# Optimization experiments

Hardware: AMD Instinct MI355X
Metric: run time of the kernel (lower is better)

Reference implementation:

```python
import jax, jax.numpy as jnp
import numpy as np
import math

PHI = (1.0 + math.sqrt(5.0)) / 2.0
LN_EPS = 1e-5


def _carrier_phases(n_heads: int) -> np.ndarray:
    """Reproduce DimensionalHeadManager._allocate carrier phases."""
    base = [k * math.pi / 7.0 for k in range(7)]  # rung base phases
    n_rungs = 7
    raw = []
    remaining = n_heads
    for i in range(n_rungs):
        if i < n_rungs - 1:
            c = max(1, round(n_heads / PHI ** (i + 1)))
            c = min(c, remaining - (n_rungs - 1 - i))
            raw.append(c)
            remaining -= c
        else:
            raw.append(max(1, remaining))
    phases = []
    for rung_idx, count in enumerate(raw):
        for j in range(count):
            phases.append(base[rung_idx] + 2.0 * math.pi / max(count, 1) * j)
    return np.asarray(phases[:n_heads], dtype=np.float32)


def setup_inputs() -> dict:
    key = jax.random.key(0)
    ks = jax.random.split(key, 7)
    B, S, D, H = 2, 2048, 1024, 16
    w_scale = 0.02  # realistic init scale for Linear weights
    x = jax.random.normal(ks[0], (B, S, D), dtype=jnp.float32)
    Wq = jax.random.normal(ks[1], (D, D), dtype=jnp.float32) * w_scale
    Wk = jax.random.normal(ks[2], (D, D), dtype=jnp.float32) * w_scale
    Wv = jax.random.normal(ks[3], (D, D), dtype=jnp.float32) * w_scale
    Wo = jax.random.normal(ks[4], (D, D), dtype=jnp.float32) * w_scale
    Wp = jax.random.normal(ks[5], (D,), dtype=jnp.float32) * w_scale  # W_phase (1,D) flattened
    gamma = jnp.ones((D,), dtype=jnp.float32)
    beta = jnp.zeros((D,), dtype=jnp.float32)
    carrier = jnp.asarray(_carrier_phases(H))  # srl.carrier_freq init
    lam = jnp.float32(0.1)  # lambda_resonance init
    return {"x": x, "Wq": Wq, "Wk": Wk, "Wv": Wv, "Wo": Wo, "Wp": Wp,
            "gamma": gamma, "beta": beta, "carrier": carrier, "lam": lam}


def reference(x, Wq, Wk, Wv, Wo, Wp, gamma, beta, carrier, lam):
    B, S, D = x.shape
    H = carrier.shape[0]
    dh = D // H
    scale = 1.0 / math.sqrt(dh)

    residual = x
    # LayerNorm
    mu = jnp.mean(x, axis=-1, keepdims=True)
    var = jnp.mean((x - mu) ** 2, axis=-1, keepdims=True)
    xn = (x - mu) * jax.lax.rsqrt(var + LN_EPS) * gamma + beta

    # Q/K/V projections (torch Linear: y = x @ W.T), split into heads
    q = jnp.einsum('bsd,ed->bse', xn, Wq).reshape(B, S, H, dh)
    k = jnp.einsum('bsd,ed->bse', xn, Wk).reshape(B, S, H, dh)
    v = jnp.einsum('bsd,ed->bse', xn, Wv).reshape(B, S, H, dh)

    # scalar phase per token, per-head carrier resonance gate
    phase = jnp.einsum('bsd,d->bs', xn, Wp)                       # (B,S)
    head_T = jnp.cos((phase[..., None] - carrier) * 0.5) ** 2     # (B,S,H)

    # attention scores + resonance term R_ij = cos^2((phi_i - phi_j)/2)
    scores = jnp.einsum('bihd,bjhd->bhij', q, k) * scale          # (B,H,S,S)
    R = jnp.cos((phase[:, :, None] - phase[:, None, :]) * 0.5) ** 2  # (B,S,S)
    scores = scores + lam * R[:, None, :, :]

    attn = jax.nn.softmax(scores, axis=-1)
    out = jnp.einsum('bhij,bjhd->bihd', attn, v)                  # (B,S,H,dh)
    out = out * head_T[..., None]                                 # per-head resonance gating
    emergent_energy = jnp.sum(jnp.abs(out))
    y = residual + jnp.einsum('bse,de->bsd', out.reshape(B, S, D), Wo)
    return (y, emergent_energy)
```

## Files before the change

kernel.cpp:

```cpp
#include <hip/hip_runtime.h>
#include <hip/hip_bf16.h>

#define S_LEN 2048
#define D_MODEL 1024
#define NH 16
#define DH 64
#define M_TOK 4096
#define DK 80
#define JS 2

typedef __attribute__((ext_vector_type(8))) short bf16x8;
typedef __attribute__((ext_vector_type(4))) float f32x4;
typedef __attribute__((ext_vector_type(16))) float f32x16;

#define LOG2E 1.4426950408889634f

__device__ __forceinline__ unsigned short f2bf(float f) {
  unsigned u = __float_as_uint(f);
  u += 0x7FFF + ((u >> 16) & 1);
  return (unsigned short)(u >> 16);
}

__device__ __forceinline__ float fexp2(float x) {
#if __has_builtin(__builtin_amdgcn_exp2f)
  return __builtin_amdgcn_exp2f(x);
#else
  float r;
  asm("v_exp_f32 %0, %1" : "=v"(r) : "v"(x));
  return r;
#endif
}

__device__ __forceinline__ void gl16(const void* g, void* l) {
  __builtin_amdgcn_global_load_lds(
      (const __attribute__((address_space(1))) unsigned int*)g,
      (__attribute__((address_space(3))) unsigned int*)l, 16, 0, 0);
}

__device__ __forceinline__ void pl32swap(unsigned int& a, unsigned int& b) {
  asm volatile("v_permlane32_swap_b32 %0, %1" : "+v"(a), "+v"(b));
}

__device__ __forceinline__ float block_sum(float v, float* sm) {
#pragma unroll
  for (int o = 32; o > 0; o >>= 1) v += __shfl_xor(v, o, 64);
  int w = threadIdx.x >> 6;
  __syncthreads();
  if ((threadIdx.x & 63) == 0) sm[w] = v;
  __syncthreads();
  return sm[0] + sm[1] + sm[2] + sm[3];
}

__global__ __launch_bounds__(256) void prep_ln_kernel(
    const float* __restrict__ Wq, const float* __restrict__ Wk,
    const float* __restrict__ Wv, const float* __restrict__ Wo,
    unsigned short* __restrict__ wbf, const float* __restrict__ x,
    const float* __restrict__ Wp, const float* __restrict__ gamma,
    const float* __restrict__ beta, unsigned short* __restrict__ xn,
    float* __restrict__ cosP, float* __restrict__ sinP,
    unsigned short* __restrict__ kk80) {
  __shared__ float sm[4];
  int bid = blockIdx.x;
  int tid = threadIdx.x;
  if (bid < 4096) {
    int idx = (bid * 256 + tid) * 4;
    int wsel = idx >> 20;
    const float* s = (wsel == 0) ? Wq : (wsel == 1) ? Wk : (wsel == 2) ? Wv : Wo;
    int off = idx & 1048575;
    float4 v = *(const float4*)(s + off);
    ushort4 p;
    p.x = f2bf(v.x); p.y = f2bf(v.y); p.z = f2bf(v.z); p.w = f2bf(v.w);
    *(ushort4*)(wbf + idx) = p;
    return;
  }
  int row = bid - 4096;
  float4 v = ((const float4*)(x + (size_t)row * D_MODEL))[tid];
  float mu = block_sum(v.x + v.y + v.z + v.w, sm) * (1.0f / D_MODEL);
  float d0 = v.x - mu, d1 = v.y - mu, d2 = v.z - mu, d3 = v.w - mu;
  float var = block_sum(d0 * d0 + d1 * d1 + d2 * d2 + d3 * d3, sm) * (1.0f / D_MODEL);
  float rinv = rsqrtf(var + 1e-5f);
  float4 g = ((const float4*)gamma)[tid];
  float4 be = ((const float4*)beta)[tid];
  float n0 = d0 * rinv * g.x + be.x;
  float n1 = d1 * rinv * g.y + be.y;
  float n2 = d2 * rinv * g.z + be.z;
  float n3 = d3 * rinv * g.w + be.w;
  ushort4 p;
  p.x = f2bf(n0); p.y = f2bf(n1); p.z = f2bf(n2); p.w = f2bf(n3);
  ((ushort4*)(xn + (size_t)row * D_MODEL))[tid] = p;
  float4 wp = ((const float4*)Wp)[tid];
  float ph = block_sum(n0 * wp.x + n1 * wp.y + n2 * wp.z + n3 * wp.w, sm);
  if (tid == 0) {
    cosP[row] = cosf(ph);
    sinP[row] = sinf(ph);
  }
  if (tid < 16) {
    float cp = cosf(ph), sp = sinf(ph);
    unsigned int w0 = (unsigned int)f2bf(cp) | ((unsigned int)f2bf(sp) << 16);
    int b_ = row >> 11, s_ = row & (S_LEN - 1);
    *(int4*)(kk80 + ((size_t)((b_ * NH + tid) * S_LEN + s_)) * DK + 64) =
        make_int4((int)w0, 0, 0, 0);
  }
}

__global__ __launch_bounds__(256, 3) void qkv_gemm_kernel(
    const unsigned short* __restrict__ xn, const unsigned short* __restrict__ wbf,
    unsigned short* __restrict__ q, unsigned short* __restrict__ kk80,
    unsigned short* __restrict__ vT) {
  __shared__ __align__(16) unsigned short As[128 * 64];
  __shared__ __align__(16) unsigned short Bs[128 * 64];
  int bid = blockIdx.x;
  bool vmode = bid >= 512;
  const unsigned short* Ap;
  const unsigned short* Bp;
  int m0, n0;
  if (!vmode) {
    m0 = (bid >> 4) * 128;
    n0 = (bid & 15) * 128;
    Ap = xn; Bp = wbf;
  } else {
    int v2 = bid - 512;
    m0 = (v2 & 7) * 128;
    n0 = (v2 >> 3) * 128;
    Ap = wbf + 2 * D_MODEL * D_MODEL; Bp = xn;
  }
  int tid = threadIdx.x;
  int wave = tid >> 6, lane = tid & 63, quad = lane >> 4, l15 = lane & 15;
  int wm = (wave & 1) * 64, wn = (wave >> 1) * 64;
  f32x4 acc[4][4];
#pragma unroll
  for (int r = 0; r < 4; ++r)
#pragma unroll
    for (int c = 0; c < 4; ++c) acc[r][c] = (f32x4){0.f, 0.f, 0.f, 0.f};

  for (int k0 = 0; k0 < D_MODEL; k0 += 64) {
    __syncthreads();
#pragma unroll
    for (int t = 0; t < 4; ++t) {
      int c = t * 256 + tid;
      int r = c >> 3, p = c & 7;
      int g = p ^ (r & 7);
      gl16(&Ap[(size_t)(m0 + r) * D_MODEL + k0 + g * 8], &As[c * 8]);
      gl16(&Bp[(size_t)(n0 + r) * D_MODEL + k0 + g * 8], &Bs[c * 8]);
    }
    __syncthreads();
    bf16x8 af[4][2], bfr[4][2];
#pragma unroll
    for (int r = 0; r < 4; ++r) {
      int R = wm + r * 16 + l15;
#pragma unroll
      for (int h = 0; h < 2; ++h)
        af[r][h] = *(const bf16x8*)&As[R * 64 + ((h * 4 + quad) ^ (R & 7)) * 8];
    }
#pragma unroll
    for (int c = 0; c < 4; ++c) {
      int R = wn + c * 16 + l15;
#pragma unroll
      for (int h = 0; h < 2; ++h)
        bfr[c][h] = *(const bf16x8*)&Bs[R * 64 + ((h * 4 + quad) ^ (R & 7)) * 8];
    }
#pragma unroll
    for (int h = 0; h < 2; ++h)
#pragma unroll
      for (int r = 0; r < 4; ++r)
#pragma unroll
        for (int c = 0; c < 4; ++c)
          acc[r][c] = __builtin_amdgcn_mfma_f32_16x16x32_bf16(af[r][h], bfr[c][h], acc[r][c], 0, 0, 0);
  }
#pragma unroll
  for (int r = 0; r < 4; ++r) {
#pragma unroll
    for (int c = 0; c < 4; ++c) {
#pragma unroll
      for (int rr = 0; rr < 4; ++rr) {
        if (vmode) {
          int e = m0 + wm + r * 16 + quad * 4 + rr;
          int tok = n0 + wn + c * 16 + l15;
          int hh = e >> 6, d = e & 63;
          int bb = tok >> 11, ss = tok & (S_LEN - 1);
          vT[(((size_t)(bb * NH + hh)) * DH + d) * S_LEN + ss] = f2bf(acc[r][c][rr]);
        } else {
          int tok = m0 + wm + r * 16 + quad * 4 + rr;
          int n = n0 + wn + c * 16 + l15;
          int e = n & 1023;
          int hh = e >> 6, d = e & 63;
          int bb = tok >> 11, ss = tok & (S_LEN - 1);
          if ((n0 >> 10) == 0) {
            q[(((size_t)(bb * NH + hh)) * S_LEN + ss) * DH + d] =
                f2bf(acc[r][c][rr] * (0.125f * LOG2E));
          } else {
            kk80[(((size_t)(bb * NH + hh)) * S_LEN + ss) * DK + d] = f2bf(acc[r][c][rr]);
          }
        }
      }
    }
  }
}

__global__ __launch_bounds__(128, 4) void attn_kernel(
    const unsigned short* __restrict__ q, const unsigned short* __restrict__ kk80,
    const unsigned short* __restrict__ vT, const float* __restrict__ cosP,
    const float* __restrict__ sinP, const float* __restrict__ lamp,
    float* __restrict__ Opart, float* __restrict__ lpart) {
  __shared__ __align__(16) unsigned short Ks[64 * 72];
  __shared__ __align__(16) unsigned short Vs[512 * 8];
  int bid = blockIdx.x;
  int slot = bid >> 3;
  int g = ((slot >> 5) << 3) | (bid & 7);
  int qt = slot & 31;
  int h = g & 15;
  int b = (g >> 4) & 1;
  int js = g >> 5;
  int bh = b * NH + h;
  int tid = threadIdx.x, wave = tid >> 6, lane = tid & 63;
  int half = lane >> 5, l31 = lane & 31;

  const unsigned short* kb = kk80 + (size_t)bh * S_LEN * DK;
  const unsigned short* vb = vT + (size_t)bh * DH * S_LEN;
  int qrow = qt * 64 + wave * 32 + l31;

  bf16x8 bQ[5];
  {
    const unsigned short* qp = q + ((size_t)bh * S_LEN + qrow) * DH;
#pragma unroll
    for (int db = 0; db < 4; ++db)
      bQ[db] = *(const bf16x8*)(qp + db * 16 + half * 8);
    bf16x8 z8 = {0, 0, 0, 0, 0, 0, 0, 0};
    if (half == 0) {
      float hl2 = 0.5f * lamp[0] * LOG2E;
      z8[0] = (short)f2bf(hl2 * cosP[b * S_LEN + qrow]);
      z8[1] = (short)f2bf(hl2 * sinP[b * S_LEN + qrow]);
    }
    bQ[4] = z8;
  }

  unsigned int cc0 = tid, cc1 = tid + 128, cc2 = tid + 256, cc3 = tid + 384,
               cc4 = tid + 512;
  unsigned int kr0 = cc0 / 9u, kr1 = cc1 / 9u, kr2 = cc2 / 9u, kr3 = cc3 / 9u,
               kr4 = cc4 / 9u;
  unsigned int ko0 = kr0 * DK + (cc0 - kr0 * 9u) * 8;
  unsigned int ko1 = kr1 * DK + (cc1 - kr1 * 9u) * 8;
  unsigned int ko2 = kr2 * DK + (cc2 - kr2 * 9u) * 8;
  unsigned int ko3 = kr3 * DK + (cc3 - kr3 * 9u) * 8;
  unsigned int ko4 = kr4 * DK + (cc4 - kr4 * 9u) * 8;
  unsigned short* kl0 = (unsigned short*)Ks + cc0 * 8;
  unsigned short* kl1 = (unsigned short*)Ks + cc1 * 8;
  unsigned short* kl2 = (unsigned short*)Ks + cc2 * 8;
  unsigned short* kl3 = (unsigned short*)Ks + cc3 * 8;
  unsigned short* kl4 = (unsigned short*)Ks + cc4 * 8;
  unsigned int vr0 = cc0 >> 3, vr1 = cc1 >> 3, vr2 = cc2 >> 3, vr3 = cc3 >> 3;
  unsigned int vo0 = vr0 * S_LEN + ((cc0 & 7) ^ (vr0 & 7)) * 8;
  unsigned int vo1 = vr1 * S_LEN + ((cc1 & 7) ^ (vr1 & 7)) * 8;
  unsigned int vo2 = vr2 * S_LEN + ((cc2 & 7) ^ (vr2 & 7)) * 8;
  unsigned int vo3 = vr3 * S_LEN + ((cc3 & 7) ^ (vr3 & 7)) * 8;
  unsigned short* vl0 = (unsigned short*)Vs + cc0 * 8;
  unsigned short* vl1 = (unsigned short*)Vs + cc1 * 8;
  unsigned short* vl2 = (unsigned short*)Vs + cc2 * 8;
  unsigned short* vl3 = (unsigned short*)Vs + cc3 * 8;

  const unsigned short* kbt = kb + (size_t)(js * (S_LEN / JS)) * DK;
  const unsigned short* vbt = vb + js * (S_LEN / JS);

  f32x16 O0 = {}, O1 = {};
  float2 l2 = {0.f, 0.f};

  for (int jt = 0; jt < S_LEN / (64 * JS); ++jt) {
    __syncthreads();
    gl16(kbt + ko0, kl0);
    gl16(kbt + ko1, kl1);
    gl16(kbt + ko2, kl2);
    gl16(kbt + ko3, kl3);
    if (tid < 64) gl16(kbt + ko4, kl4);
    gl16(vbt + vo0, vl0);
    gl16(vbt + vo1, vl1);
    gl16(vbt + vo2, vl2);
    gl16(vbt + vo3, vl3);
    kbt += 64 * DK;
    vbt += 64;
    __syncthreads();

    f32x16 Sf[2];
#pragma unroll
    for (int sj = 0; sj < 2; ++sj) {
      Sf[sj] = (f32x16){};
      int r = sj * 32 + l31;
      __builtin_amdgcn_s_setprio(1);
#pragma unroll
      for (int db = 0; db < 5; ++db) {
        int p = (db < 4) ? (db * 2 + half) : 8;
        bf16x8 aK = *(const bf16x8*)((const unsigned short*)Ks + (r * 9 + p) * 8);
        Sf[sj] = __builtin_amdgcn_mfma_f32_32x32x16_bf16(aK, bQ[db], Sf[sj], 0, 0, 0);
      }
      __builtin_amdgcn_s_setprio(0);
    }

#pragma unroll
    for (int sj = 0; sj < 2; ++sj) {
      unsigned int w[8];
#pragma unroll
      for (int rr = 0; rr < 8; ++rr) {
        float e0 = fexp2(Sf[sj][rr * 2 + 0]);
        float e1 = fexp2(Sf[sj][rr * 2 + 1]);
        l2.x += e0;
        l2.y += e1;
        __hip_bfloat162 pk2 = __float22bfloat162_rn(float2{e0, e1});
        w[rr] = *(unsigned int*)&pk2;
      }
#pragma unroll
      for (int u = 0; u < 2; ++u) {
        unsigned int a0 = w[u * 4 + 0], a1 = w[u * 4 + 1];
        unsigned int b0 = w[u * 4 + 2], b1 = w[u * 4 + 3];
        pl32swap(a0, b0);
        pl32swap(a1, b1);
        union { unsigned int u4[4]; bf16x8 v; } cvt;
        cvt.u4[0] = a0; cvt.u4[1] = a1; cvt.u4[2] = b0; cvt.u4[3] = b1;
        int jb = sj * 2 + u;
        __builtin_amdgcn_s_setprio(1);
        {
          int rv = l31;
          int p = (jb * 2 + half) ^ (rv & 7);
          bf16x8 bV = *(const bf16x8*)((const unsigned short*)Vs + (rv * 8 + p) * 8);
          O0 = __builtin_amdgcn_mfma_f32_32x32x16_bf16(cvt.v, bV, O0, 0, 0, 0);
        }
        {
          int rv = 32 + l31;
          int p = (jb * 2 + half) ^ (rv & 7);
          bf16x8 bV = *(const bf16x8*)((const unsigned short*)Vs + (rv * 8 + p) * 8);
          O1 = __builtin_amdgcn_mfma_f32_32x32x16_bf16(cvt.v, bV, O1, 0, 0, 0);
        }
        __builtin_amdgcn_s_setprio(0);
      }
    }
  }

  float l_i = l2.x + l2.y;
  l_i += __shfl_xor(l_i, 32, 64);
  size_t obase = (size_t)(js * 2 * NH + bh) * S_LEN;
#pragma unroll
  for (int reg = 0; reg < 16; ++reg) {
    int ir = (reg & 3) + 8 * (reg >> 2) + 4 * half;
    int srow = qt * 64 + wave * 32 + ir;
    Opart[((size_t)(obase + srow)) * DH + l31] = O0[reg];
    Opart[((size_t)(obase + srow)) * DH + 32 + l31] = O1[reg];
  }
  if (half == 0) lpart[obase + qt * 64 + wave * 32 + l31] = l_i;
}

__global__ __launch_bounds__(256) void combine_kernel(
    const float* __restrict__ Opart, const float* __restrict__ lpart,
    const float* __restrict__ cosP, const float* __restrict__ sinP,
    const float* __restrict__ carrier, unsigned short* __restrict__ outw,
    float* __restrict__ earray) {
  __shared__ float sm[4];
  int tok = blockIdx.x;
  int b = tok >> 11, s = tok & (S_LEN - 1);
  int t = threadIdx.x;
  int c0 = t * 4;
  int h = c0 >> 6, d0 = c0 & 63;
  int bh = b * NH + h;
  const size_t plane = (size_t)2 * NH * S_LEN;
  size_t row0 = (size_t)bh * S_LEN + s;
  float4 a0 = *(const float4*)(Opart + row0 * DH + d0);
  float4 a1 = *(const float4*)(Opart + (plane + row0) * DH + d0);
  float l = lpart[row0] + lpart[plane + row0];
  float ch = cosf(carrier[h]), sh = sinf(carrier[h]);
  float cp = cosP[tok], sp = sinP[tok];
  float gate = 0.5f + 0.5f * (cp * ch + sp * sh);
  float gl = gate / l;
  float v0 = (a0.x + a1.x) * gl, v1 = (a0.y + a1.y) * gl;
  float v2 = (a0.z + a1.z) * gl, v3 = (a0.w + a1.w) * gl;
  ushort4 p;
  p.x = f2bf(v0); p.y = f2bf(v1); p.z = f2bf(v2); p.w = f2bf(v3);
  *(ushort4*)(outw + (size_t)tok * D_MODEL + c0) = p;
  float esum = fabsf(v0) + fabsf(v1) + fabsf(v2) + fabsf(v3);
  float tot = block_sum(esum, sm);
  if (t == 0) earray[tok] = tot;
}

__global__ __launch_bounds__(256, 3) void out_gemm_kernel(
    const unsigned short* __restrict__ A, const unsigned short* __restrict__ Wo,
    const float* __restrict__ x, const float* __restrict__ earray,
    float* __restrict__ y, float* __restrict__ energy) {
  __shared__ __align__(16) unsigned short As[128 * 64];
  __shared__ __align__(16) unsigned short Bs[128 * 64];
  __shared__ float sm[4];
  int tid = threadIdx.x;
  if (blockIdx.x == 0 && blockIdx.y == 0) {
    float v = 0.f;
#pragma unroll
    for (int i = 0; i < 16; ++i) v += earray[tid + i * 256];
    float tot = block_sum(v, sm);
    if (tid == 0) *energy = tot;
  }
  int wave = tid >> 6, lane = tid & 63, quad = lane >> 4, l15 = lane & 15;
  int wm = (wave & 1) * 64, wn = (wave >> 1) * 64;
  int m0 = blockIdx.y * 128, n0 = blockIdx.x * 128;
  f32x4 acc[4][4];
#pragma unroll
  for (int r = 0; r < 4; ++r)
#pragma unroll
    for (int c = 0; c < 4; ++c) acc[r][c] = (f32x4){0.f, 0.f, 0.f, 0.f};

  for (int k0 = 0; k0 < D_MODEL; k0 += 64) {
    __syncthreads();
#pragma unroll
    for (int t = 0; t < 4; ++t) {
      int c = t * 256 + tid;
      int r = c >> 3, p = c & 7;
      int g = p ^ (r & 7);
      gl16(&A[(size_t)(m0 + r) * D_MODEL + k0 + g * 8], &As[c * 8]);
      gl16(&Wo[(size_t)(n0 + r) * D_MODEL + k0 + g * 8], &Bs[c * 8]);
    }
    __syncthreads();
    bf16x8 af[4][2], bfr[4][2];
#pragma unroll
    for (int r = 0; r < 4; ++r) {
      int R = wm + r * 16 + l15;
#pragma unroll
      for (int h = 0; h < 2; ++h)
        af[r][h] = *(const bf16x8*)&As[R * 64 + ((h * 4 + quad) ^ (R & 7)) * 8];
    }
#pragma unroll
    for (int c = 0; c < 4; ++c) {
      int R = wn + c * 16 + l15;
#pragma unroll
      for (int h = 0; h < 2; ++h)
        bfr[c][h] = *(const bf16x8*)&Bs[R * 64 + ((h * 4 + quad) ^ (R & 7)) * 8];
    }
#pragma unroll
    for (int h = 0; h < 2; ++h)
#pragma unroll
      for (int r = 0; r < 4; ++r)
#pragma unroll
        for (int c = 0; c < 4; ++c)
          acc[r][c] = __builtin_amdgcn_mfma_f32_16x16x32_bf16(af[r][h], bfr[c][h], acc[r][c], 0, 0, 0);
  }
#pragma unroll
  for (int r = 0; r < 4; ++r) {
#pragma unroll
    for (int c = 0; c < 4; ++c) {
      int dcol = n0 + wn + c * 16 + l15;
#pragma unroll
      for (int rr = 0; rr < 4; ++rr) {
        int tok = m0 + wm + r * 16 + quad * 4 + rr;
        size_t idx = (size_t)tok * D_MODEL + dcol;
        y[idx] = x[idx] + acc[r][c][rr];
      }
    }
  }
}

extern "C" void kernel_launch(void* const* d_in, const int* in_sizes, int n_in,
                              void* d_out, int out_size, void* d_ws, size_t ws_size,
                              hipStream_t stream) {
  const float* x = (const float*)d_in[0];
  const float* Wq = (const float*)d_in[1];
  const float* Wk = (const float*)d_in[2];
  const float* Wv = (const float*)d_in[3];
  const float* Wo = (const float*)d_in[4];
  const float* Wp = (const float*)d_in[5];
  const float* gamma = (const float*)d_in[6];
  const float* beta = (const float*)d_in[7];
  const float* carrier = (const float*)d_in[8];
  const float* lam = (const float*)d_in[9];

  char* ws = (char*)d_ws;
  const size_t MB = 1024 * 1024;
  unsigned short* wbf = (unsigned short*)(ws);
  unsigned short* xn = (unsigned short*)(ws + 8 * MB);
  unsigned short* qq = (unsigned short*)(ws + 16 * MB);
  unsigned short* kk80 = (unsigned short*)(ws + 24 * MB);
  unsigned short* vT = (unsigned short*)(ws + 34 * MB);
  float* cosP = (float*)(ws + 42 * MB);
  float* sinP = (float*)(ws + 42 * MB + 16 * 1024);
  float* Opart = (float*)(ws + 43 * MB);
  float* lpart = (float*)(ws + 75 * MB);
  float* earray = (float*)(ws + 76 * MB);
  unsigned short* outw = xn;

  float* y = (float*)d_out;
  float* energy = y + (out_size - 1);

  prep_ln_kernel<<<8192, 256, 0, stream>>>(Wq, Wk, Wv, Wo, wbf, x, Wp, gamma,
                                           beta, xn, cosP, sinP, kk80);
  qkv_gemm_kernel<<<768, 256, 0, stream>>>(xn, wbf, qq, kk80, vT);
  attn_kernel<<<2048, 128, 0, stream>>>(qq, kk80, vT, cosP, sinP, lam, Opart,
                                        lpart);
  combine_kernel<<<M_TOK, 256, 0, stream>>>(Opart, lpart, cosP, sinP, carrier,
                                            outw, earray);
  out_gemm_kernel<<<dim3(8, 32), 256, 0, stream>>>(outw, wbf + 3 * D_MODEL * D_MODEL,
                                                   x, earray, y, energy);
}
```

Measured before the change: 217.3 us.

## Fuse split-K combine into attention via flags; remap GEMM blocks per XCD

The separate combine kernel is removed. Each attention block writes its partial output, then bumps an atomic flag for its (bh, q-tile) pair, and the second block to arrive merges both halves, applies the head gate, writes bf16 output and a per-pair energy sum. The QKV and output GEMMs remap block indices so neighbouring M tiles land on the same XCD, and the output GEMM uses 128x64 tiles with 512 blocks. This saves a kernel launch and a pass over Opart, at the cost of a threadfence/atomic handshake whose correctness relies on the flags being zeroed in prep_ln.

```diff
diff --git a/kernel.cpp b/kernel.cpp
--- a/kernel.cpp
+++ b/kernel.cpp
@@ -58,11 +58,12 @@
     const float* __restrict__ Wp, const float* __restrict__ gamma,
     const float* __restrict__ beta, unsigned short* __restrict__ xn,
     float* __restrict__ cosP, float* __restrict__ sinP,
-    unsigned short* __restrict__ kk80) {
+    unsigned short* __restrict__ kk80, int* __restrict__ flags) {
   __shared__ float sm[4];
   int bid = blockIdx.x;
   int tid = threadIdx.x;
   if (bid < 4096) {
+    if (bid == 0) ((int4*)flags)[tid] = make_int4(0, 0, 0, 0);
     int idx = (bid * 256 + tid) * 4;
     int wsel = idx >> 20;
     const float* s = (wsel == 0) ? Wq : (wsel == 1) ? Wk : (wsel == 2) ? Wv : Wo;
@@ -115,13 +116,19 @@
   const unsigned short* Bp;
   int m0, n0;
   if (!vmode) {
-    m0 = (bid >> 4) * 128;
-    n0 = (bid & 15) * 128;
+    int xcd = bid & 7, slot = bid >> 3;
+    int n = slot & 15, mh = slot >> 4;
+    int m = (mh << 3) | xcd;
+    m0 = m * 128;
+    n0 = n * 128;
     Ap = xn; Bp = wbf;
   } else {
-    int v2 = bid - 512;
-    m0 = (v2 & 7) * 128;
-    n0 = (v2 >> 3) * 128;
+    int b2 = bid - 512;
+    int xcd = b2 & 7, slot = b2 >> 3;
+    int m = slot & 7, nh = slot >> 3;
+    int n = (nh << 3) | xcd;
+    m0 = m * 128;
+    n0 = n * 128;
     Ap = wbf + 2 * D_MODEL * D_MODEL; Bp = xn;
   }
   int tid = threadIdx.x;
@@ -200,10 +207,14 @@
 __global__ __launch_bounds__(128, 4) void attn_kernel(
     const unsigned short* __restrict__ q, const unsigned short* __restrict__ kk80,
     const unsigned short* __restrict__ vT, const float* __restrict__ cosP,
-    const float* __restrict__ sinP, const float* __restrict__ lamp,
-    float* __restrict__ Opart, float* __restrict__ lpart) {
+    const float* __restrict__ sinP, const float* __restrict__ carrier,
+    const float* __restrict__ lamp, float* __restrict__ Opart,
+    float* __restrict__ lpart, unsigned short* __restrict__ outw,
+    float* __restrict__ earray, int* __restrict__ flags) {
   __shared__ __align__(16) unsigned short Ks[64 * 72];
   __shared__ __align__(16) unsigned short Vs[512 * 8];
+  __shared__ float Lr[2][32];
+  __shared__ float er[4];
   int bid = blockIdx.x;
   int slot = bid >> 3;
   int g = ((slot >> 5) << 3) | (bid & 7);
@@ -335,46 +346,47 @@
 
   float l_i = l2.x + l2.y;
   l_i += __shfl_xor(l_i, 32, 64);
+  Lr[wave][l31] = l_i;
   size_t obase = (size_t)(js * 2 * NH + bh) * S_LEN;
 #pragma unroll
   for (int reg = 0; reg < 16; ++reg) {
     int ir = (reg & 3) + 8 * (reg >> 2) + 4 * half;
     int srow = qt * 64 + wave * 32 + ir;
-    Opart[((size_t)(obase + srow)) * DH + l31] = O0[reg];
-    Opart[((size_t)(obase + srow)) * DH + 32 + l31] = O1[reg];
+    Opart[(obase + srow) * DH + l31] = O0[reg];
+    Opart[(obase + srow) * DH + 32 + l31] = O1[reg];
   }
   if (half == 0) lpart[obase + qt * 64 + wave * 32 + l31] = l_i;
-}
-
-__global__ __launch_bounds__(256) void combine_kernel(
-    const float* __restrict__ Opart, const float* __restrict__ lpart,
-    const float* __restrict__ cosP, const float* __restrict__ sinP,
-    const float* __restrict__ carrier, unsigned short* __restrict__ outw,
-    float* __restrict__ earray) {
-  __shared__ float sm[4];
-  int tok = blockIdx.x;
-  int b = tok >> 11, s = tok & (S_LEN - 1);
-  int t = threadIdx.x;
-  int c0 = t * 4;
-  int h = c0 >> 6, d0 = c0 & 63;
-  int bh = b * NH + h;
-  const size_t plane = (size_t)2 * NH * S_LEN;
-  size_t row0 = (size_t)bh * S_LEN + s;
-  float4 a0 = *(const float4*)(Opart + row0 * DH + d0);
-  float4 a1 = *(const float4*)(Opart + (plane + row0) * DH + d0);
-  float l = lpart[row0] + lpart[plane + row0];
+  __threadfence();
+  __syncthreads();
+  int pair = bh * 32 + qt;
+  if (tid == 0) er[0] = (float)atomicAdd(&flags[pair], 1);
+  __syncthreads();
+  if (er[0] < 0.5f) return;
+  __threadfence();
+
+  size_t pbase = (size_t)((1 - js) * 2 * NH + bh) * S_LEN;
   float ch = cosf(carrier[h]), sh = sinf(carrier[h]);
-  float cp = cosP[tok], sp = sinP[tok];
-  float gate = 0.5f + 0.5f * (cp * ch + sp * sh);
-  float gl = gate / l;
-  float v0 = (a0.x + a1.x) * gl, v1 = (a0.y + a1.y) * gl;
-  float v2 = (a0.z + a1.z) * gl, v3 = (a0.w + a1.w) * gl;
-  ushort4 p;
-  p.x = f2bf(v0); p.y = f2bf(v1); p.z = f2bf(v2); p.w = f2bf(v3);
-  *(ushort4*)(outw + (size_t)tok * D_MODEL + c0) = p;
-  float esum = fabsf(v0) + fabsf(v1) + fabsf(v2) + fabsf(v3);
-  float tot = block_sum(esum, sm);
-  if (t == 0) earray[tok] = tot;
+  float esum = 0.f;
+#pragma unroll
+  for (int reg = 0; reg < 16; ++reg) {
+    int ir = (reg & 3) + 8 * (reg >> 2) + 4 * half;
+    int srow = qt * 64 + wave * 32 + ir;
+    float lT = Lr[wave][ir] + lpart[pbase + srow];
+    float cp = cosP[b * S_LEN + srow], sp = sinP[b * S_LEN + srow];
+    float gate = 0.5f + 0.5f * (cp * ch + sp * sh);
+    float gl = gate / lT;
+    float v0 = (O0[reg] + Opart[(pbase + srow) * DH + l31]) * gl;
+    float v1 = (O1[reg] + Opart[(pbase + srow) * DH + 32 + l31]) * gl;
+    esum += fabsf(v0) + fabsf(v1);
+    size_t tok = (size_t)b * S_LEN + srow;
+    outw[tok * D_MODEL + h * DH + l31] = f2bf(v0);
+    outw[tok * D_MODEL + h * DH + 32 + l31] = f2bf(v1);
+  }
+#pragma unroll
+  for (int off = 32; off > 0; off >>= 1) esum += __shfl_xor(esum, off, 64);
+  if (lane == 0) er[2 + wave] = esum;
+  __syncthreads();
+  if (tid == 0) earray[pair] = er[2] + er[3];
 }
 
 __global__ __launch_bounds__(256, 3) void out_gemm_kernel(
@@ -382,24 +394,26 @@
     const float* __restrict__ x, const float* __restrict__ earray,
     float* __restrict__ y, float* __restrict__ energy) {
   __shared__ __align__(16) unsigned short As[128 * 64];
-  __shared__ __align__(16) unsigned short Bs[128 * 64];
+  __shared__ __align__(16) unsigned short Bs[64 * 64];
   __shared__ float sm[4];
   int tid = threadIdx.x;
-  if (blockIdx.x == 0 && blockIdx.y == 0) {
-    float v = 0.f;
-#pragma unroll
-    for (int i = 0; i < 16; ++i) v += earray[tid + i * 256];
+  int bid = blockIdx.x;
+  if (bid == 0) {
+    float v = earray[tid] + earray[tid + 256] + earray[tid + 512] + earray[tid + 768];
     float tot = block_sum(v, sm);
     if (tid == 0) *energy = tot;
   }
+  int xcd = bid & 7, slot = bid >> 3;
+  int n = slot & 15, mh = slot >> 4;
+  int m = (mh << 3) | xcd;
+  int m0 = m * 128, n0 = n * 64;
   int wave = tid >> 6, lane = tid & 63, quad = lane >> 4, l15 = lane & 15;
-  int wm = (wave & 1) * 64, wn = (wave >> 1) * 64;
-  int m0 = blockIdx.y * 128, n0 = blockIdx.x * 128;
-  f32x4 acc[4][4];
+  int wm = (wave & 1) * 64, wn = (wave >> 1) * 32;
+  f32x4 acc[4][2];
 #pragma unroll
   for (int r = 0; r < 4; ++r)
 #pragma unroll
-    for (int c = 0; c < 4; ++c) acc[r][c] = (f32x4){0.f, 0.f, 0.f, 0.f};
+    for (int c = 0; c < 2; ++c) acc[r][c] = (f32x4){0.f, 0.f, 0.f, 0.f};
 
   for (int k0 = 0; k0 < D_MODEL; k0 += 64) {
     __syncthreads();
@@ -407,12 +421,18 @@
     for (int t = 0; t < 4; ++t) {
       int c = t * 256 + tid;
       int r = c >> 3, p = c & 7;
-      int g = p ^ (r & 7);
-      gl16(&A[(size_t)(m0 + r) * D_MODEL + k0 + g * 8], &As[c * 8]);
-      gl16(&Wo[(size_t)(n0 + r) * D_MODEL + k0 + g * 8], &Bs[c * 8]);
+      int qc = p ^ (r & 7);
+      gl16(&A[(size_t)(m0 + r) * D_MODEL + k0 + qc * 8], &As[c * 8]);
+    }
+#pragma unroll
+    for (int t = 0; t < 2; ++t) {
+      int c = t * 256 + tid;
+      int r = c >> 3, p = c & 7;
+      int qc = p ^ (r & 7);
+      gl16(&Wo[(size_t)(n0 + r) * D_MODEL + k0 + qc * 8], &Bs[c * 8]);
     }
     __syncthreads();
-    bf16x8 af[4][2], bfr[4][2];
+    bf16x8 af[4][2], bfr[2][2];
 #pragma unroll
     for (int r = 0; r < 4; ++r) {
       int R = wm + r * 16 + l15;
@@ -421,7 +441,7 @@
         af[r][h] = *(const bf16x8*)&As[R * 64 + ((h * 4 + quad) ^ (R & 7)) * 8];
     }
 #pragma unroll
-    for (int c = 0; c < 4; ++c) {
+    for (int c = 0; c < 2; ++c) {
       int R = wn + c * 16 + l15;
 #pragma unroll
       for (int h = 0; h < 2; ++h)
@@ -432,13 +452,13 @@
 #pragma unroll
       for (int r = 0; r < 4; ++r)
 #pragma unroll
-        for (int c = 0; c < 4; ++c)
+        for (int c = 0; c < 2; ++c)
           acc[r][c] = __builtin_amdgcn_mfma_f32_16x16x32_bf16(af[r][h], bfr[c][h], acc[r][c], 0, 0, 0);
   }
 #pragma unroll
   for (int r = 0; r < 4; ++r) {
 #pragma unroll
-    for (int c = 0; c < 4; ++c) {
+    for (int c = 0; c < 2; ++c) {
       int dcol = n0 + wn + c * 16 + l15;
 #pragma unroll
       for (int rr = 0; rr < 4; ++rr) {
@@ -476,18 +496,17 @@
   float* Opart = (float*)(ws + 43 * MB);
   float* lpart = (float*)(ws + 75 * MB);
   float* earray = (float*)(ws + 76 * MB);
+  int* flags = (int*)(ws + 76 * MB + 8 * 1024);
   unsigned short* outw = xn;
 
   float* y = (float*)d_out;
   float* energy = y + (out_size - 1);
 
   prep_ln_kernel<<<8192, 256, 0, stream>>>(Wq, Wk, Wv, Wo, wbf, x, Wp, gamma,
-                                           beta, xn, cosP, sinP, kk80);
+                                           beta, xn, cosP, sinP, kk80, flags);
   qkv_gemm_kernel<<<768, 256, 0, stream>>>(xn, wbf, qq, kk80, vT);
-  attn_kernel<<<2048, 128, 0, stream>>>(qq, kk80, vT, cosP, sinP, lam, Opart,
-                                        lpart);
-  combine_kernel<<<M_TOK, 256, 0, stream>>>(Opart, lpart, cosP, sinP, carrier,
-                                            outw, earray);
-  out_gemm_kernel<<<dim3(8, 32), 256, 0, stream>>>(outw, wbf + 3 * D_MODEL * D_MODEL,
-                                                   x, earray, y, energy);
-}
+  attn_kernel<<<2048, 128, 0, stream>>>(qq, kk80, vT, cosP, sinP, carrier, lam,
+                                        Opart, lpart, outw, earray, flags);
+  out_gemm_kernel<<<512, 256, 0, stream>>>(outw, wbf + 3 * D_MODEL * D_MODEL,
+                                           x, earray, y, energy);
+}
```

Measured after the change: 382.5 us. +76.0%, slower.
